# Kernel optimization log

Measured on AMD Instinct MI355X. Metric: run time of the kernel, lower is better.

## Reference

```python
import jax, jax.numpy as jnp
import numpy as np

N_NODES = 40000
N_EDGES = 640000
D_IN = 128
D_OUT = 128
ALPHA = 0.5   # real-valued complex alpha from init
Q = 0.25      # magnetic potential parameter


def setup_inputs() -> dict:
    key = jax.random.key(0)
    k = jax.random.split(key, 6)
    x = jax.random.normal(k[0], (N_NODES, D_IN), dtype=jnp.float32)
    edge_index = jax.random.randint(k[1], (2, N_EDGES), 0, N_NODES, dtype=jnp.int32)
    W1 = jax.random.normal(k[2], (D_IN, D_OUT), dtype=jnp.float32) * 0.05
    b1 = jax.random.normal(k[3], (D_OUT,), dtype=jnp.float32) * 0.05
    W2 = jax.random.normal(k[4], (D_IN, D_OUT), dtype=jnp.float32) * 0.05
    b2 = jax.random.normal(k[5], (D_OUT,), dtype=jnp.float32) * 0.05
    return {"x": x, "edge_index": edge_index, "W1": W1, "b1": b1, "W2": W2, "b2": b2}


def _magnet_spmm(x, edge_index, q):
    """y = H @ x where H = D_s^{-1/2} (A_s * exp(i*2*pi*q*(A - A^T))) D_s^{-1/2},
    A_s = 0.5*(A + A^T). Returns (y_real, y_imag); x is real (zero imag part)."""
    n = x.shape[0]
    row, col = edge_index[0], edge_index[1]
    e = row.shape[0]
    # detect whether the reverse edge (col,row) exists in the edge set
    keys = row * n + col
    rkeys = col * n + row
    sk = jnp.sort(keys)
    pos = jnp.searchsorted(sk, rkeys)
    has_rev = (pos < e) & (sk[jnp.clip(pos, 0, e - 1)] == rkeys)
    # symmetrize: each directed edge contributes 0.5 in both directions.
    # forward copy carries phase sign +1, reversed copy sign -1; phase is 0
    # when both directions exist (A - A^T = 0 there).
    r_all = jnp.concatenate([row, col])          # [2E]
    c_all = jnp.concatenate([col, row])
    sign = jnp.concatenate([jnp.ones((e,), x.dtype), -jnp.ones((e,), x.dtype)])
    hr = jnp.concatenate([has_rev, has_rev]).astype(x.dtype)
    theta = (2.0 * np.pi * q) * sign * (1.0 - hr)
    half = jnp.asarray(0.5, x.dtype)
    # symmetrized degree: deg[u] = sum_v A_s[u,v]
    deg = jax.ops.segment_sum(jnp.full((2 * e,), 0.5, x.dtype), r_all, num_segments=n)
    dinv = jnp.where(deg > 0, 1.0 / jnp.sqrt(deg), 0.0)
    scale = half * dinv[r_all] * dinv[c_all]
    val_re = scale * jnp.cos(theta)
    val_im = scale * jnp.sin(theta)
    xg = x[c_all]                                # [2E, D] gather
    y_re = jax.ops.segment_sum(val_re[:, None] * xg, r_all, num_segments=n)
    y_im = jax.ops.segment_sum(val_im[:, None] * xg, r_all, num_segments=n)
    return y_re, y_im


def reference(x, edge_index, W1, b1, W2, b2):
    y_re, y_im = _magnet_spmm(x, edge_index, Q)
    # alpha * lin1(y) + (1-alpha) * lin2(y), applied to real and imag parts
    out_re = ALPHA * (y_re @ W1 + b1) + (1.0 - ALPHA) * (y_re @ W2 + b2)
    out_im = ALPHA * (y_im @ W1 + b1) + (1.0 - ALPHA) * (y_im @ W2 + b2)
    return jnp.concatenate([out_re, out_im], axis=1)  # [N, 2*D_OUT]
```

## Files before the change

### kernel.cpp

```cpp
#include <hip/hip_runtime.h>
#include <math.h>

#define N_NODES 40000
#define D 128
#define NEDGE 640000
#define CAP 80
#define PB 1250

__device__ __forceinline__ unsigned short bf16rn(float f) {
    unsigned u = __float_as_uint(f);
    unsigned r = u + 0x7FFFu + ((u >> 16) & 1u);
    return (unsigned short)(r >> 16);
}

__global__ void init_kernel(int* __restrict__ cursorA, int* __restrict__ cursorB,
                            const float* __restrict__ W1, const float* __restrict__ W2,
                            float* __restrict__ Wc) {
    int i = blockIdx.x * blockDim.x + threadIdx.x;
    int stride = gridDim.x * blockDim.x;
    for (int t = i; t < N_NODES; t += stride) { cursorA[t] = 0; cursorB[t] = 0; }
    for (int t = i; t < D * D; t += stride) Wc[t] = 0.5f * (W1[t] + W2[t]);
}

__global__ __launch_bounds__(256) void prep_kernel(
    const int* __restrict__ row, const int* __restrict__ col,
    int* __restrict__ cursorA, int* __restrict__ cursorB,
    unsigned short* __restrict__ entries,
    const float* __restrict__ x, const float* __restrict__ Wc,
    unsigned short* __restrict__ z) {
    int bid = blockIdx.x, tid = threadIdx.x;

    int e0 = bid * 512 + tid, e1 = e0 + 256;
    int r0 = row[e0], c0 = col[e0];
    int r1 = row[e1], c1 = col[e1];
    int pa0 = atomicAdd(&cursorA[r0], 1);
    int pb0 = atomicAdd(&cursorB[c0], 1);
    int pa1 = atomicAdd(&cursorA[r1], 1);
    int pb1 = atomicAdd(&cursorB[c1], 1);

    int c4 = tid & 31;
    const float4* Wv = (const float4*)Wc;
    for (int pass = 0; pass < 4; ++pass) {
        int node = bid * 32 + pass * 8 + (tid >> 5);
        const float* xr = x + (size_t)node * D;
        float4 acc = make_float4(0.f, 0.f, 0.f, 0.f);
        #pragma unroll 4
        for (int k = 0; k < D; ++k) {
            float xv = xr[k];
            float4 w = Wv[k * 32 + c4];
            acc.x += xv * w.x; acc.y += xv * w.y;
            acc.z += xv * w.z; acc.w += xv * w.w;
        }
        ushort4 o;
        o.x = bf16rn(acc.x); o.y = bf16rn(acc.y);
        o.z = bf16rn(acc.z); o.w = bf16rn(acc.w);
        ((ushort4*)(z + (size_t)node * D))[c4] = o;
    }

    if (pa0 < CAP) entries[(size_t)r0 * CAP + pa0] = (unsigned short)c0;
    if (pb0 < CAP) entries[(size_t)c0 * CAP + (CAP - 1 - pb0)] = (unsigned short)r0;
    if (pa1 < CAP) entries[(size_t)r1 * CAP + pa1] = (unsigned short)c1;
    if (pb1 < CAP) entries[(size_t)c1 * CAP + (CAP - 1 - pb1)] = (unsigned short)r1;
}

__global__ __launch_bounds__(256) void gather_kernel(
    const unsigned short* __restrict__ z, const unsigned short* __restrict__ entries,
    const int* __restrict__ cursorA, const int* __restrict__ cursorB,
    const float* __restrict__ b1, const float* __restrict__ b2,
    float* __restrict__ out) {
    __shared__ unsigned short rawlds[4][2][CAP];
    __shared__ uint2 slds[4][2][CAP];

    int tid = threadIdx.x;
    int wave = tid >> 6, half = (tid >> 5) & 1, l = tid & 31;
    int n = wave * 2 + half;
    int u = blockIdx.x * 8 + n;

    int cA = cursorA[u], cB = cursorB[u];
    int a = min(cA, CAP);
    int b = min(cB, CAP - a);
    int m = a + b;
    int cnt = cA + cB;
    float dinv_u = (cnt > 0) ? rsqrtf(0.5f * (float)cnt) : 0.f;
    const unsigned short* eb = entries + (size_t)u * CAP;
    int gap = CAP - m;

    for (int t = l; t < m; t += 32)
        rawlds[wave][half][t] = eb[t < a ? t : t + gap];
    __builtin_amdgcn_wave_barrier();

    for (int t = l; t < m; t += 32) {
        unsigned short src = rawlds[wave][half][t];
        bool d1 = (t >= a);
        int lo = d1 ? 0 : a, hi = d1 ? a : m;
        bool rev = false;
        for (int j = lo; j < hi; ++j)
            rev |= (rawlds[wave][half][j] == src);
        int cs = cursorA[src] + cursorB[src];
        float s = 0.5f * dinv_u * rsqrtf(0.5f * (float)max(cs, 1));
        unsigned flag = 0u;
        float sval;
        if (rev) { sval = s; flag = 0x10000u; }
        else     { sval = d1 ? -s : s; }
        slds[wave][half][t] = make_uint2((unsigned)src | flag, __float_as_uint(sval));
    }
    __builtin_amdgcn_wave_barrier();

    float4 accre = make_float4(0.f, 0.f, 0.f, 0.f);
    float4 accim = make_float4(0.f, 0.f, 0.f, 0.f);

    #pragma unroll 8
    for (int i = 0; i < m; ++i) {
        uint2 t = slds[wave][half][i];
        unsigned src = t.x & 0xFFFFu;
        float s = __uint_as_float(t.y);
        bool isre = (t.x & 0x10000u) != 0u;
        float fre = isre ? s : 0.f;
        float fim = isre ? 0.f : s;
        uint2 v = ((const uint2*)(z + (size_t)src * D))[l];
        float v0 = __uint_as_float(v.x << 16);
        float v1 = __uint_as_float(v.x & 0xFFFF0000u);
        float v2 = __uint_as_float(v.y << 16);
        float v3 = __uint_as_float(v.y & 0xFFFF0000u);
        accre.x += fre * v0; accre.y += fre * v1;
        accre.z += fre * v2; accre.w += fre * v3;
        accim.x += fim * v0; accim.y += fim * v1;
        accim.z += fim * v2; accim.w += fim * v3;
    }

    float4 ba = ((const float4*)b1)[l];
    float4 bb = ((const float4*)b2)[l];
    float4 bv = make_float4(0.5f * (ba.x + bb.x), 0.5f * (ba.y + bb.y),
                            0.5f * (ba.z + bb.z), 0.5f * (ba.w + bb.w));
    accre.x += bv.x; accre.y += bv.y; accre.z += bv.z; accre.w += bv.w;
    accim.x += bv.x; accim.y += bv.y; accim.z += bv.z; accim.w += bv.w;

    *(float4*)&out[(size_t)u * 256 + l * 4] = accre;
    *(float4*)&out[(size_t)u * 256 + 128 + l * 4] = accim;
}

extern "C" void kernel_launch(void* const* d_in, const int* in_sizes, int n_in,
                              void* d_out, int out_size, void* d_ws, size_t ws_size,
                              hipStream_t stream) {
    const float* x  = (const float*)d_in[0];
    const int*   ei = (const int*)d_in[1];
    const float* W1 = (const float*)d_in[2];
    const float* b1 = (const float*)d_in[3];
    const float* W2 = (const float*)d_in[4];
    const float* b2 = (const float*)d_in[5];
    float* out = (float*)d_out;
    const int* row = ei;
    const int* col = ei + NEDGE;

    char* ws = (char*)d_ws;
    float*          Wc      = (float*)ws;
    int*            cursorA = (int*)(ws + 65536);
    int*            cursorB = (int*)(ws + 225536);
    unsigned short* entries = (unsigned short*)(ws + 385536);
    unsigned short* z       = (unsigned short*)(ws + 6785536);

    init_kernel<<<512, 256, 0, stream>>>(cursorA, cursorB, W1, W2, Wc);
    prep_kernel<<<PB, 256, 0, stream>>>(row, col, cursorA, cursorB, entries, x, Wc, z);
    gather_kernel<<<N_NODES / 8, 256, 0, stream>>>(z, entries, cursorA, cursorB, b1, b2, out);
}
```

Measured before the change: 205.0 us.

## Restructure prep kernel: stage x rows in LDS and compute 8 outputs per thread

```diff
diff --git a/kernel.cpp b/kernel.cpp
--- a/kernel.cpp
+++ b/kernel.cpp
@@ -5,7 +5,7 @@
 #define D 128
 #define NEDGE 640000
 #define CAP 80
-#define PB 1250
+#define WB 2500
 
 __device__ __forceinline__ unsigned short bf16rn(float f) {
     unsigned u = __float_as_uint(f);
@@ -22,45 +22,53 @@
     for (int t = i; t < D * D; t += stride) Wc[t] = 0.5f * (W1[t] + W2[t]);
 }
 
-__global__ __launch_bounds__(256) void prep_kernel(
+__global__ __launch_bounds__(256) void work_kernel(
     const int* __restrict__ row, const int* __restrict__ col,
     int* __restrict__ cursorA, int* __restrict__ cursorB,
     unsigned short* __restrict__ entries,
     const float* __restrict__ x, const float* __restrict__ Wc,
     unsigned short* __restrict__ z) {
+    __shared__ float xl[16][129];
     int bid = blockIdx.x, tid = threadIdx.x;
 
-    int e0 = bid * 512 + tid, e1 = e0 + 256;
-    int r0 = row[e0], c0 = col[e0];
-    int r1 = row[e1], c1 = col[e1];
-    int pa0 = atomicAdd(&cursorA[r0], 1);
-    int pb0 = atomicAdd(&cursorB[c0], 1);
-    int pa1 = atomicAdd(&cursorA[r1], 1);
-    int pb1 = atomicAdd(&cursorB[c1], 1);
+    int e = bid * 256 + tid;
+    int r = row[e], c = col[e];
+    int p1 = atomicAdd(&cursorA[r], 1);
+    if (p1 < CAP) entries[(size_t)r * CAP + p1] = (unsigned short)c;
+    int p2 = atomicAdd(&cursorB[c], 1);
+    if (p2 < CAP) entries[(size_t)c * CAP + (CAP - 1 - p2)] = (unsigned short)r;
 
-    int c4 = tid & 31;
+    int node0 = bid * 16;
+    const float4* xs = (const float4*)(x + (size_t)node0 * D);
+    #pragma unroll
+    for (int t = tid; t < 16 * 32; t += 256)
+        *(float4*)&xl[t >> 5][(t & 31) * 4] = xs[t];
+    __syncthreads();
+
+    int ng = tid >> 4;
+    int c8 = tid & 15;
+    float acc[8];
+    #pragma unroll
+    for (int j = 0; j < 8; ++j) acc[j] = 0.f;
+
     const float4* Wv = (const float4*)Wc;
-    for (int pass = 0; pass < 4; ++pass) {
-        int node = bid * 32 + pass * 8 + (tid >> 5);
-        const float* xr = x + (size_t)node * D;
-        float4 acc = make_float4(0.f, 0.f, 0.f, 0.f);
-        #pragma unroll 4
-        for (int k = 0; k < D; ++k) {
-            float xv = xr[k];
-            float4 w = Wv[k * 32 + c4];
-            acc.x += xv * w.x; acc.y += xv * w.y;
-            acc.z += xv * w.z; acc.w += xv * w.w;
-        }
-        ushort4 o;
-        o.x = bf16rn(acc.x); o.y = bf16rn(acc.y);
-        o.z = bf16rn(acc.z); o.w = bf16rn(acc.w);
-        ((ushort4*)(z + (size_t)node * D))[c4] = o;
+    #pragma unroll 4
+    for (int k = 0; k < D; ++k) {
+        float4 wa = Wv[k * 32 + c8 * 2];
+        float4 wb = Wv[k * 32 + c8 * 2 + 1];
+        float xv = xl[ng][k];
+        acc[0] += xv * wa.x; acc[1] += xv * wa.y;
+        acc[2] += xv * wa.z; acc[3] += xv * wa.w;
+        acc[4] += xv * wb.x; acc[5] += xv * wb.y;
+        acc[6] += xv * wb.z; acc[7] += xv * wb.w;
     }
-
-    if (pa0 < CAP) entries[(size_t)r0 * CAP + pa0] = (unsigned short)c0;
-    if (pb0 < CAP) entries[(size_t)c0 * CAP + (CAP - 1 - pb0)] = (unsigned short)r0;
-    if (pa1 < CAP) entries[(size_t)r1 * CAP + pa1] = (unsigned short)c1;
-    if (pb1 < CAP) entries[(size_t)c1 * CAP + (CAP - 1 - pb1)] = (unsigned short)r1;
+    ushort4 o1, o2;
+    o1.x = bf16rn(acc[0]); o1.y = bf16rn(acc[1]);
+    o1.z = bf16rn(acc[2]); o1.w = bf16rn(acc[3]);
+    o2.x = bf16rn(acc[4]); o2.y = bf16rn(acc[5]);
+    o2.z = bf16rn(acc[6]); o2.w = bf16rn(acc[7]);
+    ushort4* zp = (ushort4*)(z + (size_t)(node0 + ng) * D + c8 * 8);
+    zp[0] = o1; zp[1] = o2;
 }
 
 __global__ __launch_bounds__(256) void gather_kernel(
@@ -160,6 +168,6 @@
     unsigned short* z       = (unsigned short*)(ws + 6785536);
 
     init_kernel<<<512, 256, 0, stream>>>(cursorA, cursorB, W1, W2, Wc);
-    prep_kernel<<<PB, 256, 0, stream>>>(row, col, cursorA, cursorB, entries, x, Wc, z);
+    work_kernel<<<WB, 256, 0, stream>>>(row, col, cursorA, cursorB, entries, x, Wc, z);
     gather_kernel<<<N_NODES / 8, 256, 0, stream>>>(z, entries, cursorA, cursorB, b1, b2, out);
 }
```

Measured after the change: 181.9 us. -11.2%, faster.
